# Kernel optimization log

Hardware: AMD Instinct MI355X
Metric: run time of the kernel (lower is better)

Reference implementation:

```python
import jax, jax.numpy as jnp
import numpy as np

B, V, K, DIN, H, DH, OBS, HID = 2048, 3, 32, 256, 8, 64, 128, 256
REP = H * DH
EPS = 1e-6


def _ln(x, g, b):
    mu = x.mean(-1, keepdims=True)
    var = ((x - mu) ** 2).mean(-1, keepdims=True)
    return (x - mu) * jax.lax.rsqrt(var + 1e-5) * g + b


def setup_inputs() -> dict:
    key = jax.random.key(0)
    ks = iter(jax.random.split(key, 32))
    nrm = lambda shape, s=0.05: jax.random.normal(next(ks), shape, jnp.float32) * s
    return {
        'x_anchor': jax.random.normal(next(ks), (B, V, DIN), jnp.float32),
        'x_neighbors': jax.random.normal(next(ks), (B, V, K, DIN), jnp.float32),
        'edge_weights': jax.random.uniform(next(ks), (B, V, K), jnp.float32),
        'g': jax.random.normal(next(ks), (B, OBS), jnp.float32),
        'aW': nrm((V, DIN, REP)), 'ab': jnp.zeros((V, REP)), 'ag': jnp.ones((V, REP)), 'abeta': jnp.zeros((V, REP)),
        'nW': nrm((V, DIN, REP)), 'nb': jnp.zeros((V, REP)), 'ng': jnp.ones((V, REP)), 'nbeta': jnp.zeros((V, REP)),
        'Wq': nrm((V, H, DH, DH)), 'Wk': nrm((V, H, DH, DH)), 'Wv': nrm((V, H, DH, DH)), 'Wo': nrm((V, H, DH, DH)),
        'geom_log_scale': jnp.zeros((V, H)),
        'cWq': nrm((H, DH, DH)), 'cWk': nrm((H, DH, DH)), 'cWv': nrm((H, DH, DH)), 'cWo': nrm((H, DH, DH)),
        'rW1': nrm((OBS, HID)), 'rb1': jnp.zeros((HID,)),
        'rW2': nrm((HID, HID)), 'rb2': jnp.zeros((HID,)),
        'vW': nrm((HID, H * V)), 'vb': jnp.zeros((H * V,)),
        'mW': nrm((HID, H)), 'mb': jnp.zeros((H,)),
        'gW': nrm((HID, H)), 'gb': jnp.zeros((H,)),
    }


def reference(x_anchor, x_neighbors, edge_weights, g, aW, ab, ag, abeta, nW, nb, ng, nbeta,
              Wq, Wk, Wv, Wo, geom_log_scale, cWq, cWk, cWv, cWo,
              rW1, rb1, rW2, rb2, vW, vb, mW, mb, gW, gb):
    # --- per-view encoders (vectorized over V with a leading v axis) ---
    ha = _ln(jnp.einsum('bvi,vio->bvo', x_anchor, aW) + ab, ag, abeta).reshape(B, V, H, DH)
    hn = _ln(jnp.einsum('bvki,vio->bvko', x_neighbors, nW) + nb[:, None, :],
             ng[:, None, :], nbeta[:, None, :]).reshape(B, V, K, H, DH)
    q = jnp.einsum('bvhd,vhde->bvhe', ha, Wq)
    k = jnp.einsum('bvkhd,vhde->bvkhe', hn, Wk)
    vv = jnp.einsum('bvkhd,vhde->bvkhe', hn, Wv)
    sc = jnp.einsum('bvhd,bvkhd->bvhk', q, k) / np.sqrt(DH).astype(np.float32)
    geom = jax.nn.softplus(geom_log_scale)  # [V,H]
    sc = sc + geom[None, :, :, None] * jnp.log(edge_weights[:, :, None, :] + EPS)
    attn = jax.nn.softmax(sc, axis=-1)
    ho = jnp.einsum('bvhk,bvkhd->bvhd', attn, vv)
    ho = jnp.einsum('bvhd,vhde->bvhe', ho, Wo) + ha  # residual
    view_tokens = jnp.transpose(ho, (0, 2, 1, 3))  # [B,H,V,Dh]
    # --- router ---
    hid = jax.nn.gelu(jnp.dot(g, rW1) + rb1, approximate=False)
    hid = jax.nn.gelu(jnp.dot(hid, rW2) + rb2, approximate=False)
    pi = jax.nn.softmax((jnp.dot(hid, vW) + vb).reshape(B, H, V), axis=-1)
    beta = jax.nn.sigmoid((jnp.dot(hid, mW) + mb)[..., None])  # [B,H,1]
    gate = jax.nn.softmax(jnp.dot(hid, gW) + gb, axis=-1)      # [B,H]
    # --- pi-weighted mixture + cross-view interaction with log-pi prior ---
    mix = jnp.einsum('bhv,bhvd->bhd', pi, view_tokens)
    qc = jnp.einsum('bhd,hde->bhe', mix, cWq)
    kc = jnp.einsum('bhvd,hde->bhve', view_tokens, cWk)
    vc = jnp.einsum('bhvd,hde->bhve', view_tokens, cWv)
    s2 = jnp.einsum('bhd,bhvd->bhv', qc, kc) / np.sqrt(DH).astype(np.float32) + jnp.log(pi + EPS)
    a2 = jax.nn.softmax(s2, axis=-1)
    cr = jnp.einsum('bhv,bhvd->bhd', a2, vc)
    cr = jnp.einsum('bhd,hde->bhe', cr, cWo)
    # mode blend + head gating; head_repr kept unflattened [B,H,Dh]
    return gate[..., None] * (beta * cr + (1.0 - beta) * mix)
```

## Files before the change

### kernel.cpp

```cpp
#include <hip/hip_runtime.h>

#define B_   2048
#define V_   3
#define K_   32
#define DIN_ 256
#define H_   8
#define DH_  64
#define REP_ 512

typedef unsigned short u16;
typedef unsigned int   u32;
typedef __bf16 bf8 __attribute__((ext_vector_type(8)));
typedef float  f4  __attribute__((ext_vector_type(4)));

static __device__ __forceinline__ u16 f2bf(float f) {
  union { float f; u32 i; } x; x.f = f;
  u32 r = (x.i + 0x7FFFu + ((x.i >> 16) & 1u)) >> 16;
  return (u16)r;
}
static __device__ __forceinline__ float bf2f(u16 u) {
  union { u32 i; float f; } x; x.i = ((u32)u) << 16;
  return x.f;
}
static __device__ __forceinline__ float bflo(u32 q) {
  union { u32 i; float f; } x; x.i = q << 16; return x.f;
}
static __device__ __forceinline__ float bfhi(u32 q) {
  union { u32 i; float f; } x; x.i = q & 0xffff0000u; return x.f;
}

static __device__ __forceinline__ void gl2lds16(const u16* g, u16* l) {
  __builtin_amdgcn_global_load_lds(
      (const __attribute__((address_space(1))) unsigned int*)(g),
      (__attribute__((address_space(3))) unsigned int*)(l), 16, 0, 0);
}

__global__ __launch_bounds__(256) void k0_prep(
    const float* __restrict__ nW, const float* __restrict__ aW,
    const float* __restrict__ Wv,
    u16* __restrict__ nWt, u16* __restrict__ aWt,
    u16* __restrict__ Wvt)
{
  int id = blockIdx.x * 256 + threadIdx.x;
  if (id < 393216) {
    int v  = id / 131072, r  = id % 131072;
    int kt = r / 16384,   r2 = r % 16384;
    int n  = r2 >> 5;
    int s  = (r2 >> 3) & 3;
    int m  = r2 & 7;
    int c  = s ^ ((n >> 1) & 3);
    int k  = kt * 32 + c * 8 + m;
    int src = (v * 256 + k) * 512 + n;
    nWt[id] = f2bf(nW[src]);
    aWt[id] = f2bf(aW[src]);
  } else {
    int j = id - 393216;
    int vh = j / 4096, r = j % 4096;
    int e = r / 64, d = r % 64;
    int src = (vh * 64 + d) * 64 + e;
    Wvt[j] = f2bf(Wv[src]);
  }
}

__global__ __launch_bounds__(256) void k0_wqk(
    const float* __restrict__ Wq, const float* __restrict__ Wk,
    float* __restrict__ Wqk)
{
  int vh = blockIdx.x, t = threadIdx.x;
  __shared__ float wq[4096], wkT[4096];
  #pragma unroll
  for (int i = 0; i < 16; ++i) {
    int idx = i * 256 + t;
    wq[idx] = Wq[(long)vh * 4096 + idx];
    int e = idx >> 6, c = idx & 63;
    wkT[c * 64 + e] = Wk[(long)vh * 4096 + e * 64 + c];
  }
  __syncthreads();
  int d = t >> 2, e0 = (t & 3) * 16;
  float acc[16];
  #pragma unroll
  for (int j = 0; j < 16; ++j) acc[j] = 0.f;
  for (int c = 0; c < 64; ++c) {
    float a = wq[d * 64 + c];
    const float* wr = &wkT[c * 64 + e0];
    #pragma unroll
    for (int j = 0; j < 16; ++j) acc[j] += a * wr[j];
  }
  #pragma unroll
  for (int j = 0; j < 16; ++j) Wqk[(long)vh * 4096 + d * 64 + e0 + j] = acc[j];
}

__global__ __launch_bounds__(256) void k_tq(
    const float* __restrict__ ha, const float* __restrict__ Wqk,
    float* __restrict__ tB)
{
  __shared__ float hs[512];
  int bv = blockIdx.x, t = threadIdx.x;
  int v = bv % 3;
  hs[t]       = ha[(long)bv * 512 + t];
  hs[256 + t] = ha[(long)bv * 512 + 256 + t];
  __syncthreads();
  int h = t >> 5, e0 = (t & 31) * 2;
  const float* wq = Wqk + ((long)v * 8 + h) * 4096 + e0;
  const float* hv = &hs[h * 64];
  float a0 = 0.f, a1 = 0.f;
  #pragma unroll 4
  for (int d = 0; d < 64; ++d) {
    float x = hv[d];
    float2 wv = *(const float2*)&wq[d * 64];
    a0 += x * wv.x;
    a1 += x * wv.y;
  }
  tB[(long)bv * 512 + h * 64 + e0]     = a0 * 0.125f;
  tB[(long)bv * 512 + h * 64 + e0 + 1] = a1 * 0.125f;
}

union K1Smem {
  struct { u16 A[64 * 256]; u16 B[16384]; } p;
  u16 S[64 * 512];
};

__global__ __launch_bounds__(512, 4) void k1_gemm_ln(
    const float* __restrict__ X,
    const u16*   __restrict__ Wt,
    const float* __restrict__ bias,
    const float* __restrict__ gamma,
    const float* __restrict__ betap,
    u16*   __restrict__ hn,
    float* __restrict__ ha,
    int mode, int b0, int Bc)
{
  __shared__ K1Smem sm;
  const int v = blockIdx.y, blk = blockIdx.x, t = threadIdx.x;
  const int w = t >> 6, l = t & 63, lm = l & 15, lg = l >> 4;
  const int wm = w & 1, wn = w >> 1;

  float bcol[8];
  #pragma unroll
  for (int tn = 0; tn < 8; ++tn) bcol[tn] = bias[v * 512 + wn * 128 + tn * 16 + lm];

  {
    int row = t >> 3;
    int cbase = (t & 7) * 32;
    long grow;
    if (mode == 0) { int b = b0 + blk * 2 + (row >> 5); grow = ((long)(b * 3 + v) * 32 + (row & 31)) * 256; }
    else           { int b = blk * 64 + row;            grow = (long)(b * 3 + v) * 256; }
    const float4* src = (const float4*)(X + grow + cbase);
    int sw = row & 7;
    #pragma unroll
    for (int j = 0; j < 8; ++j) {
      float4 f = src[j];
      int col = cbase + j * 4;
      int c = col >> 3, m = col & 7;
      ushort4 u;
      u.x = f2bf(f.x); u.y = f2bf(f.y); u.z = f2bf(f.z); u.w = f2bf(f.w);
      *(ushort4*)&sm.p.A[row * 256 + ((c ^ sw) << 3) + m] = u;
    }
  }

  f4 acc[2][8];
  #pragma unroll
  for (int i = 0; i < 2; ++i)
    #pragma unroll
    for (int j = 0; j < 8; ++j) { f4 z = {0.f, 0.f, 0.f, 0.f}; acc[i][j] = z; }

  const u16* Wbase = Wt + (long)v * 8 * 16384;
  for (int kt = 0; kt < 8; ++kt) {
    __syncthreads();
    {
      const u16* gp = Wbase + (long)kt * 16384 + t * 8;
      u16* lp = &sm.p.B[t * 8];
      #pragma unroll
      for (int r = 0; r < 4; ++r) gl2lds16(gp + r * 4096, lp + r * 4096);
    }
    __syncthreads();
    bf8 af[2];
    #pragma unroll
    for (int tm = 0; tm < 2; ++tm) {
      int row = wm * 32 + tm * 16 + lm;
      int c = kt * 4 + lg;
      af[tm] = *(const bf8*)&sm.p.A[row * 256 + ((c ^ (row & 7)) << 3)];
    }
    #pragma unroll
    for (int tn = 0; tn < 8; ++tn) {
      int n = wn * 128 + tn * 16 + lm;
      bf8 bv = *(const bf8*)&sm.p.B[n * 32 + ((lg ^ ((n >> 1) & 3)) << 3)];
      acc[0][tn] = __builtin_amdgcn_mfma_f32_16x16x32_bf16(af[0], bv, acc[0][tn], 0, 0, 0);
      acc[1][tn] = __builtin_amdgcn_mfma_f32_16x16x32_bf16(af[1], bv, acc[1][tn], 0, 0, 0);
    }
  }
  __syncthreads();

  #pragma unroll
  for (int tm = 0; tm < 2; ++tm)
    #pragma unroll
    for (int tn = 0; tn < 8; ++tn) {
      int col = wn * 128 + tn * 16 + lm;
      int c = col >> 3, m = col & 7;
      #pragma unroll
      for (int r = 0; r < 4; ++r) {
        int row = wm * 32 + tm * 16 + lg * 4 + r;
        sm.S[row * 512 + ((c ^ (row & 7)) << 3) + m] = f2bf(acc[tm][tn][r] + bcol[tn]);
      }
    }
  __syncthreads();

  {
    int row = t >> 3, ch = t & 7, sw = row & 7;
    float s1 = 0.f, s2 = 0.f;
    #pragma unroll
    for (int j = 0; j < 8; ++j) {
      int c = j * 8 + ch;
      uint4 q = *(const uint4*)&sm.S[row * 512 + ((c ^ sw) << 3)];
      float x0 = bflo(q.x), x1 = bfhi(q.x), x2 = bflo(q.y), x3 = bfhi(q.y);
      float x4 = bflo(q.z), x5 = bfhi(q.z), x6 = bflo(q.w), x7 = bfhi(q.w);
      s1 += ((x0 + x1) + (x2 + x3)) + ((x4 + x5) + (x6 + x7));
      s2 += ((x0*x0 + x1*x1) + (x2*x2 + x3*x3)) + ((x4*x4 + x5*x5) + (x6*x6 + x7*x7));
    }
    #pragma unroll
    for (int d = 1; d < 8; d <<= 1) { s1 += __shfl_xor(s1, d, 64); s2 += __shfl_xor(s2, d, 64); }
    float mu = s1 * (1.f / 512.f);
    float var = s2 * (1.f / 512.f) - mu * mu;
    float rs = rsqrtf(var + 1e-5f);
    #pragma unroll
    for (int j = 0; j < 8; ++j) {
      int c = j * 8 + ch;
      uint4 q = *(const uint4*)&sm.S[row * 512 + ((c ^ sw) << 3)];
      int col0 = c * 8;
      float4 g0 = *(const float4*)&gamma[v * 512 + col0];
      float4 g1 = *(const float4*)&gamma[v * 512 + col0 + 4];
      float4 e0 = *(const float4*)&betap[v * 512 + col0];
      float4 e1 = *(const float4*)&betap[v * 512 + col0 + 4];
      float y0 = (bflo(q.x) - mu) * rs * g0.x + e0.x;
      float y1 = (bfhi(q.x) - mu) * rs * g0.y + e0.y;
      float y2 = (bflo(q.y) - mu) * rs * g0.z + e0.z;
      float y3 = (bfhi(q.y) - mu) * rs * g0.w + e0.w;
      float y4 = (bflo(q.z) - mu) * rs * g1.x + e1.x;
      float y5 = (bfhi(q.z) - mu) * rs * g1.y + e1.y;
      float y6 = (bflo(q.w) - mu) * rs * g1.z + e1.z;
      float y7 = (bfhi(q.w) - mu) * rs * g1.w + e1.w;
      if (mode == 0) {
        uint4 q4;
        q4.x = (u32)f2bf(y0) | ((u32)f2bf(y1) << 16);
        q4.y = (u32)f2bf(y2) | ((u32)f2bf(y3) << 16);
        q4.z = (u32)f2bf(y4) | ((u32)f2bf(y5) << 16);
        q4.w = (u32)f2bf(y6) | ((u32)f2bf(y7) << 16);
        int bl_ = blk * 2 + (row >> 5), krow = row & 31;
        u16* dst = hn + (((long)(v * 8 + j) * Bc + bl_) * 32 + krow) * 64 + ch * 8;
        *(uint4*)dst = q4;
      } else {
        int b = blk * 64 + row;
        float* dst = ha + (long)(b * 3 + v) * 512 + col0;
        float4 w0, w1;
        w0.x = y0; w0.y = y1; w0.z = y2; w0.w = y3;
        w1.x = y4; w1.y = y5; w1.z = y6; w1.w = y7;
        *(float4*)dst = w0;
        *(float4*)(dst + 4) = w1;
      }
    }
  }
}

__global__ __launch_bounds__(512, 4) void k12_fused(
    const float* __restrict__ X,
    const u16*   __restrict__ Wt,
    const float* __restrict__ bias,
    const float* __restrict__ gamma,
    const float* __restrict__ betap,
    const float* __restrict__ ha,
    const u16*   __restrict__ Wvt,
    const float* __restrict__ tB,
    const float* __restrict__ Wo,
    const float* __restrict__ ew,
    const float* __restrict__ gls,
    float* __restrict__ vt)
{
  __shared__ K1Smem sm;
  __shared__ float tS[1024];
  __shared__ float aS[512];
  __shared__ float oS[1024];
  __shared__ float haS[1024];

  const int v = blockIdx.y, blk = blockIdx.x, t = threadIdx.x;
  const int w = t >> 6, l = t & 63, lm = l & 15, lg = l >> 4;
  const int wm = w & 1, wn = w >> 1;

  float bcol[8];
  #pragma unroll
  for (int tn = 0; tn < 8; ++tn) bcol[tn] = bias[v * 512 + wn * 128 + tn * 16 + lm];

  {
    int row = t >> 3;
    int cbase = (t & 7) * 32;
    int b = blk * 2 + (row >> 5);
    long grow = ((long)(b * 3 + v) * 32 + (row & 31)) * 256;
    const float4* src = (const float4*)(X + grow + cbase);
    int sw = row & 7;
    #pragma unroll
    for (int j = 0; j < 8; ++j) {
      float4 f = src[j];
      int col = cbase + j * 4;
      int c = col >> 3, m = col & 7;
      ushort4 u;
      u.x = f2bf(f.x); u.y = f2bf(f.y); u.z = f2bf(f.z); u.w = f2bf(f.w);
      *(ushort4*)&sm.p.A[row * 256 + ((c ^ sw) << 3) + m] = u;
    }
  }
  {
    int b = t >> 8, e = (t & 255) * 2;
    *(float2*)&haS[b * 512 + e] =
        *(const float2*)&ha[((long)(blk * 2 + b) * 3 + v) * 512 + e];
    *(float2*)&tS[b * 512 + e] =
        *(const float2*)&tB[((long)(blk * 2 + b) * 3 + v) * 512 + e];
  }

  f4 acc[2][8];
  #pragma unroll
  for (int i = 0; i < 2; ++i)
    #pragma unroll
    for (int j = 0; j < 8; ++j) { f4 z = {0.f, 0.f, 0.f, 0.f}; acc[i][j] = z; }

  const u16* Wbase = Wt + (long)v * 8 * 16384;
  for (int kt = 0; kt < 8; ++kt) {
    __syncthreads();
    {
      const u16* gp = Wbase + (long)kt * 16384 + t * 8;
      u16* lp = &sm.p.B[t * 8];
      #pragma unroll
      for (int r = 0; r < 4; ++r) gl2lds16(gp + r * 4096, lp + r * 4096);
    }
    __syncthreads();
    bf8 af[2];
    #pragma unroll
    for (int tm = 0; tm < 2; ++tm) {
      int row = wm * 32 + tm * 16 + lm;
      int c = kt * 4 + lg;
      af[tm] = *(const bf8*)&sm.p.A[row * 256 + ((c ^ (row & 7)) << 3)];
    }
    #pragma unroll
    for (int tn = 0; tn < 8; ++tn) {
      int n = wn * 128 + tn * 16 + lm;
      bf8 bv = *(const bf8*)&sm.p.B[n * 32 + ((lg ^ ((n >> 1) & 3)) << 3)];
      acc[0][tn] = __builtin_amdgcn_mfma_f32_16x16x32_bf16(af[0], bv, acc[0][tn], 0, 0, 0);
      acc[1][tn] = __builtin_amdgcn_mfma_f32_16x16x32_bf16(af[1], bv, acc[1][tn], 0, 0, 0);
    }
  }
  __syncthreads();

  #pragma unroll
  for (int tm = 0; tm < 2; ++tm)
    #pragma unroll
    for (int tn = 0; tn < 8; ++tn) {
      int col = wn * 128 + tn * 16 + lm;
      int c = col >> 3, m = col & 7;
      #pragma unroll
      for (int r = 0; r < 4; ++r) {
        int row = wm * 32 + tm * 16 + lg * 4 + r;
        sm.S[row * 512 + ((c ^ (row & 7)) << 3) + m] = f2bf(acc[tm][tn][r] + bcol[tn]);
      }
    }
  __syncthreads();

  {
    int row = t >> 3, ch = t & 7, sw = row & 7;
    float s1 = 0.f, s2 = 0.f;
    #pragma unroll
    for (int j = 0; j < 8; ++j) {
      int c = j * 8 + ch;
      uint4 q = *(const uint4*)&sm.S[row * 512 + ((c ^ sw) << 3)];
      float x0 = bflo(q.x), x1 = bfhi(q.x), x2 = bflo(q.y), x3 = bfhi(q.y);
      float x4 = bflo(q.z), x5 = bfhi(q.z), x6 = bflo(q.w), x7 = bfhi(q.w);
      s1 += ((x0 + x1) + (x2 + x3)) + ((x4 + x5) + (x6 + x7));
      s2 += ((x0*x0 + x1*x1) + (x2*x2 + x3*x3)) + ((x4*x4 + x5*x5) + (x6*x6 + x7*x7));
    }
    #pragma unroll
    for (int d = 1; d < 8; d <<= 1) { s1 += __shfl_xor(s1, d, 64); s2 += __shfl_xor(s2, d, 64); }
    float mu = s1 * (1.f / 512.f);
    float var = s2 * (1.f / 512.f) - mu * mu;
    float rs = rsqrtf(var + 1e-5f);
    #pragma unroll
    for (int j = 0; j < 8; ++j) {
      int c = j * 8 + ch;
      u16* sp = &sm.S[row * 512 + ((c ^ sw) << 3)];
      uint4 q = *(const uint4*)sp;
      int col0 = c * 8;
      float4 g0 = *(const float4*)&gamma[v * 512 + col0];
      float4 g1 = *(const float4*)&gamma[v * 512 + col0 + 4];
      float4 e0 = *(const float4*)&betap[v * 512 + col0];
      float4 e1 = *(const float4*)&betap[v * 512 + col0 + 4];
      float y0 = (bflo(q.x) - mu) * rs * g0.x + e0.x;
      float y1 = (bfhi(q.x) - mu) * rs * g0.y + e0.y;
      float y2 = (bflo(q.y) - mu) * rs * g0.z + e0.z;
      float y3 = (bfhi(q.y) - mu) * rs * g0.w + e0.w;
      float y4 = (bflo(q.z) - mu) * rs * g1.x + e1.x;
      float y5 = (bfhi(q.z) - mu) * rs * g1.y + e1.y;
      float y6 = (bflo(q.w) - mu) * rs * g1.z + e1.z;
      float y7 = (bfhi(q.w) - mu) * rs * g1.w + e1.w;
      uint4 q4;
      q4.x = (u32)f2bf(y0) | ((u32)f2bf(y1) << 16);
      q4.y = (u32)f2bf(y2) | ((u32)f2bf(y3) << 16);
      q4.z = (u32)f2bf(y4) | ((u32)f2bf(y5) << 16);
      q4.w = (u32)f2bf(y6) | ((u32)f2bf(y7) << 16);
      *(uint4*)sp = q4;
    }
  }
  __syncthreads();

  {
    int b = t >> 8, h = (t >> 5) & 7, k = t & 31;
    float x = gls[v * 8 + h];
    float gsc = (x > 20.f) ? x : log1pf(expf(x));
    int r = b * 32 + k, sw = r & 7;
    const float* tb = &tS[(b * 8 + h) * 64];
    float s = 0.f;
    #pragma unroll
    for (int j = 0; j < 8; ++j) {
      int c8 = h * 8 + j;
      uint4 q = *(const uint4*)&sm.S[r * 512 + ((c8 ^ sw) << 3)];
      const float* tj = tb + j * 8;
      s += tj[0] * bflo(q.x) + tj[1] * bfhi(q.x)
         + tj[2] * bflo(q.y) + tj[3] * bfhi(q.y)
         + tj[4] * bflo(q.z) + tj[5] * bfhi(q.z)
         + tj[6] * bflo(q.w) + tj[7] * bfhi(q.w);
    }
    float e_w = ew[((long)(blk * 2 + b) * 3 + v) * 32 + k];
    s += gsc * logf(e_w + 1e-6f);
    float m = s;
    #pragma unroll
    for (int d = 1; d < 32; d <<= 1) m = fmaxf(m, __shfl_xor(m, d, 64));
    float exs = expf(s - m), sum = exs;
    #pragma unroll
    for (int d = 1; d < 32; d <<= 1) sum += __shfl_xor(sum, d, 64);
    aS[(b * 8 + h) * 32 + k] = exs / sum;
  }
  __syncthreads();

  #pragma unroll 1
  for (int i = 0; i < 2; ++i) {
    int p = w * 2 + i, b = p >> 3, h = p & 7;
    const u16* wvg = Wvt + (long)(v * 8 + h) * 4096;
    f4 aV[2][4];
    #pragma unroll
    for (int a = 0; a < 2; ++a)
      #pragma unroll
      for (int j = 0; j < 4; ++j) { f4 z = {0.f, 0.f, 0.f, 0.f}; aV[a][j] = z; }
    #pragma unroll
    for (int ks = 0; ks < 2; ++ks) {
      int ko = ks * 32 + lg * 8;
      bf8 af[2];
      #pragma unroll
      for (int tm = 0; tm < 2; ++tm) {
        int r = b * 32 + tm * 16 + lm;
        int c8 = h * 8 + ks * 4 + lg;
        af[tm] = *(const bf8*)&sm.S[r * 512 + ((c8 ^ (r & 7)) << 3)];
      }
      #pragma unroll
      for (int tn = 0; tn < 4; ++tn) {
        bf8 bv = *(const bf8*)&wvg[(tn * 16 + lm) * 64 + ko];
        #pragma unroll
        for (int tm = 0; tm < 2; ++tm)
          aV[tm][tn] = __builtin_amdgcn_mfma_f32_16x16x32_bf16(af[tm], bv, aV[tm][tn], 0, 0, 0);
      }
    }
    float pp[4] = {0.f, 0.f, 0.f, 0.f};
    #pragma unroll
    for (int tm = 0; tm < 2; ++tm)
      #pragma unroll
      for (int r4 = 0; r4 < 4; ++r4) {
        int k = tm * 16 + lg * 4 + r4;
        float a = aS[p * 32 + k];
        #pragma unroll
        for (int tn = 0; tn < 4; ++tn) pp[tn] += a * aV[tm][tn][r4];
      }
    #pragma unroll
    for (int tn = 0; tn < 4; ++tn) {
      float x = pp[tn];
      x += __shfl_xor(x, 16, 64);
      x += __shfl_xor(x, 32, 64);
      if (l < 16) oS[p * 64 + tn * 16 + lm] = x;
    }
  }
  __syncthreads();

  {
    int h = t >> 6, e = t & 63;
    const float* wo = Wo + (long)(v * 8 + h) * 4096;
    float a0 = haS[h * 64 + e];
    float a1 = haS[512 + h * 64 + e];
    const float* o0 = &oS[h * 64];
    const float* o1 = &oS[512 + h * 64];
    #pragma unroll 4
    for (int d = 0; d < 64; ++d) {
      float wv = wo[d * 64 + e];
      a0 += o0[d] * wv;
      a1 += o1[d] * wv;
    }
    vt[(((long)(blk * 2 + 0) * 8 + h) * 3 + v) * 64 + e] = a0;
    vt[(((long)(blk * 2 + 1) * 8 + h) * 3 + v) * 64 + e] = a1;
  }
}

__global__ __launch_bounds__(256) void k3_router(
    const float* __restrict__ g, const float* __restrict__ rW1, const float* __restrict__ rb1,
    const float* __restrict__ rW2, const float* __restrict__ rb2,
    const float* __restrict__ vW, const float* __restrict__ vb,
    const float* __restrict__ mW, const float* __restrict__ mb,
    const float* __restrict__ gW, const float* __restrict__ gb,
    float* __restrict__ pi, float* __restrict__ beta_o, float* __restrict__ gate_o)
{
  __shared__ float gs[4 * 128], h1[4 * 256], h2[4 * 256], lgt[4 * 40];
  int t = threadIdx.x, bb = blockIdx.x * 4;
  #pragma unroll
  for (int r = 0; r < 2; ++r) { int idx = r * 256 + t; gs[idx] = g[(long)bb * 128 + idx]; }
  __syncthreads();
  {
    int bl = t >> 6, e0 = (t & 63) * 4;
    float acc[4];
    #pragma unroll
    for (int j = 0; j < 4; ++j) acc[j] = rb1[e0 + j];
    for (int i = 0; i < 128; ++i) {
      float gv = gs[bl * 128 + i];
      const float* wr = rW1 + i * 256 + e0;
      #pragma unroll
      for (int j = 0; j < 4; ++j) acc[j] += gv * wr[j];
    }
    #pragma unroll
    for (int j = 0; j < 4; ++j) { float x = acc[j]; h1[bl * 256 + e0 + j] = 0.5f * x * (1.f + erff(x * 0.70710678118f)); }
  }
  __syncthreads();
  {
    int bl = t >> 6, e0 = (t & 63) * 4;
    float acc[4];
    #pragma unroll
    for (int j = 0; j < 4; ++j) acc[j] = rb2[e0 + j];
    for (int i = 0; i < 256; ++i) {
      float hv = h1[bl * 256 + i];
      const float* wr = rW2 + i * 256 + e0;
      #pragma unroll
      for (int j = 0; j < 4; ++j) acc[j] += hv * wr[j];
    }
    #pragma unroll
    for (int j = 0; j < 4; ++j) { float x = acc[j]; h2[bl * 256 + e0 + j] = 0.5f * x * (1.f + erff(x * 0.70710678118f)); }
  }
  __syncthreads();
  if (t < 160) {
    int bl = t / 40, j = t % 40;
    const float* W; float bs; int col, stride;
    if (j < 24)      { W = vW; col = j;      stride = 24; bs = vb[j]; }
    else if (j < 32) { W = mW; col = j - 24; stride = 8;  bs = mb[j - 24]; }
    else             { W = gW; col = j - 32; stride = 8;  bs = gb[j - 32]; }
    float acc = bs;
    for (int i = 0; i < 256; ++i) acc += h2[bl * 256 + i] * W[i * stride + col];
    lgt[bl * 40 + j] = acc;
  }
  __syncthreads();
  if (t < 4) {
    int b = bb + t;
    const float* L = &lgt[t * 40];
    #pragma unroll
    for (int hh = 0; hh < 8; ++hh) {
      float a0 = L[hh * 3], a1 = L[hh * 3 + 1], a2v = L[hh * 3 + 2];
      float m = fmaxf(a0, fmaxf(a1, a2v));
      float x0 = expf(a0 - m), x1 = expf(a1 - m), x2 = expf(a2v - m);
      float inv = 1.f / (x0 + x1 + x2);
      pi[b * 24 + hh * 3 + 0] = x0 * inv;
      pi[b * 24 + hh * 3 + 1] = x1 * inv;
      pi[b * 24 + hh * 3 + 2] = x2 * inv;
      beta_o[b * 8 + hh] = 1.f / (1.f + expf(-L[24 + hh]));
    }
    float m = L[32];
    #pragma unroll
    for (int hh = 1; hh < 8; ++hh) m = fmaxf(m, L[32 + hh]);
    float s = 0.f, ex[8];
    #pragma unroll
    for (int hh = 0; hh < 8; ++hh) { ex[hh] = expf(L[32 + hh] - m); s += ex[hh]; }
    float inv = 1.f / s;
    #pragma unroll
    for (int hh = 0; hh < 8; ++hh) gate_o[b * 8 + hh] = ex[hh] * inv;
  }
}

__global__ __launch_bounds__(256) void k4_cross(
    const float* __restrict__ vtg, const float* __restrict__ pig,
    const float* __restrict__ betag, const float* __restrict__ gateg,
    const float* __restrict__ cWq, const float* __restrict__ cWk,
    const float* __restrict__ cWv, const float* __restrict__ cWo,
    float* __restrict__ out)
{
  __shared__ float smem[12544];
  float* vts   = smem;
  float* mixs  = smem + 6144;
  float* buf1  = smem + 8192;
  float* buf2  = smem + 10240;
  float* a2s   = smem + 12288;
  float* pis   = smem + 12384;
  float* betas = smem + 12480;
  float* gates = smem + 12512;

  int t = threadIdx.x, bblk = blockIdx.x * 4;
  {
    const float4* src = (const float4*)(vtg + (long)bblk * 1536);
    #pragma unroll
    for (int r = 0; r < 6; ++r) ((float4*)vts)[r * 256 + t] = src[r * 256 + t];
    if (t < 96) pis[t] = pig[bblk * 24 + t];
    if (t < 32) { betas[t] = betag[bblk * 8 + t]; gates[t] = gateg[bblk * 8 + t]; }
  }
  __syncthreads();
  int bl = t >> 6, hh = (t >> 3) & 7, e0 = (t & 7) * 8;
  const float* vbh = &vts[(bl * 8 + hh) * 192];
  {
    float p0 = pis[bl * 24 + hh * 3], p1 = pis[bl * 24 + hh * 3 + 1], p2 = pis[bl * 24 + hh * 3 + 2];
    #pragma unroll
    for (int j = 0; j < 8; ++j) {
      int e = e0 + j;
      mixs[(bl * 8 + hh) * 64 + e] = p0 * vbh[e] + p1 * vbh[64 + e] + p2 * vbh[128 + e];
    }
  }
  __syncthreads();
  {
    float acc[8] = {0.f,0.f,0.f,0.f,0.f,0.f,0.f,0.f};
    const float* M = &mixs[(bl * 8 + hh) * 64];
    for (int d = 0; d < 64; ++d) {
      float mv = M[d];
      const float* wr = &cWq[(hh * 64 + d) * 64 + e0];
      #pragma unroll
      for (int j = 0; j < 8; ++j) acc[j] += mv * wr[j];
    }
    #pragma unroll
    for (int j = 0; j < 8; ++j) buf1[(bl * 8 + hh) * 64 + e0 + j] = acc[j] * 0.125f;
  }
  __syncthreads();
  {
    const float* Q = &buf1[(bl * 8 + hh) * 64];
    #pragma unroll
    for (int d2 = 0; d2 < 8; ++d2) {
      const float* wr = &cWk[(hh * 64 + e0 + d2) * 64];
      float a = 0.f;
      for (int e = 0; e < 64; ++e) a += wr[e] * Q[e];
      buf2[(bl * 8 + hh) * 64 + e0 + d2] = a;
    }
  }
  __syncthreads();
  if (t < 32) {
    int b2 = t >> 3, h2 = t & 7;
    const float* Wd = &buf2[(b2 * 8 + h2) * 64];
    const float* vb2 = &vts[(b2 * 8 + h2) * 192];
    float s[3];
    #pragma unroll
    for (int v3 = 0; v3 < 3; ++v3) {
      float a = 0.f;
      for (int d = 0; d < 64; ++d) a += Wd[d] * vb2[v3 * 64 + d];
      s[v3] = a + logf(pis[b2 * 24 + h2 * 3 + v3] + 1e-6f);
    }
    float m = fmaxf(s[0], fmaxf(s[1], s[2]));
    float x0 = expf(s[0] - m), x1 = expf(s[1] - m), x2 = expf(s[2] - m);
    float inv = 1.f / (x0 + x1 + x2);
    a2s[(b2 * 8 + h2) * 3 + 0] = x0 * inv;
    a2s[(b2 * 8 + h2) * 3 + 1] = x1 * inv;
    a2s[(b2 * 8 + h2) * 3 + 2] = x2 * inv;
  }
  __syncthreads();
  {
    float a0 = a2s[(bl * 8 + hh) * 3], a1 = a2s[(bl * 8 + hh) * 3 + 1], a2v = a2s[(bl * 8 + hh) * 3 + 2];
    #pragma unroll
    for (int j = 0; j < 8; ++j) {
      int e = e0 + j;
      buf1[(bl * 8 + hh) * 64 + e] = a0 * vbh[e] + a1 * vbh[64 + e] + a2v * vbh[128 + e];
    }
  }
  __syncthreads();
  {
    float acc[8] = {0.f,0.f,0.f,0.f,0.f,0.f,0.f,0.f};
    const float* Y = &buf1[(bl * 8 + hh) * 64];
    for (int d = 0; d < 64; ++d) {
      float yv = Y[d];
      const float* wr = &cWv[(hh * 64 + d) * 64 + e0];
      #pragma unroll
      for (int j = 0; j < 8; ++j) acc[j] += yv * wr[j];
    }
    #pragma unroll
    for (int j = 0; j < 8; ++j) buf2[(bl * 8 + hh) * 64 + e0 + j] = acc[j];
  }
  __syncthreads();
  {
    float acc[8] = {0.f,0.f,0.f,0.f,0.f,0.f,0.f,0.f};
    const float* C2 = &buf2[(bl * 8 + hh) * 64];
    for (int d = 0; d < 64; ++d) {
      float cv = C2[d];
      const float* wr = &cWo[(hh * 64 + d) * 64 + e0];
      #pragma unroll
      for (int j = 0; j < 8; ++j) acc[j] += cv * wr[j];
    }
    float bt = betas[bl * 8 + hh], gt = gates[bl * 8 + hh];
    const float* M = &mixs[(bl * 8 + hh) * 64];
    #pragma unroll
    for (int j = 0; j < 8; ++j)
      out[((long)(bblk + bl) * 8 + hh) * 64 + e0 + j] = gt * (bt * acc[j] + (1.f - bt) * M[e0 + j]);
  }
}

extern "C" void kernel_launch(void* const* d_in, const int* in_sizes, int n_in,
                              void* d_out, int out_size, void* d_ws, size_t ws_size,
                              hipStream_t stream) {
  const float* x_anchor    = (const float*)d_in[0];
  const float* x_neighbors = (const float*)d_in[1];
  const float* edge_w      = (const float*)d_in[2];
  const float* g           = (const float*)d_in[3];
  const float* aW  = (const float*)d_in[4];
  const float* ab  = (const float*)d_in[5];
  const float* ag  = (const float*)d_in[6];
  const float* abeta = (const float*)d_in[7];
  const float* nW  = (const float*)d_in[8];
  const float* nb  = (const float*)d_in[9];
  const float* ng  = (const float*)d_in[10];
  const float* nbeta = (const float*)d_in[11];
  const float* Wq  = (const float*)d_in[12];
  const float* Wk  = (const float*)d_in[13];
  const float* Wv  = (const float*)d_in[14];
  const float* Wo  = (const float*)d_in[15];
  const float* gls = (const float*)d_in[16];
  const float* cWq = (const float*)d_in[17];
  const float* cWk = (const float*)d_in[18];
  const float* cWv = (const float*)d_in[19];
  const float* cWo = (const float*)d_in[20];
  const float* rW1 = (const float*)d_in[21];
  const float* rb1 = (const float*)d_in[22];
  const float* rW2 = (const float*)d_in[23];
  const float* rb2 = (const float*)d_in[24];
  const float* vW  = (const float*)d_in[25];
  const float* vb  = (const float*)d_in[26];
  const float* mW  = (const float*)d_in[27];
  const float* mb  = (const float*)d_in[28];
  const float* gW  = (const float*)d_in[29];
  const float* gb  = (const float*)d_in[30];

  char* p = (char*)d_ws;
  u16* nWt = (u16*)p;  p += 786432;
  u16* aWt = (u16*)p;  p += 786432;
  u16* Wvt = (u16*)p;  p += 196608;
  float* WqkB = (float*)p; p += 393216;
  float* ha   = (float*)p; p += 12582912;
  float* vtb  = (float*)p; p += 12582912;
  float* tqB  = (float*)p; p += 12582912;
  float* pib  = (float*)p; p += 196608;
  float* betb = (float*)p; p += 65536;
  float* gatb = (float*)p; p += 65536;
  (void)ws_size;

  k0_prep<<<1920, 256, 0, stream>>>(nW, aW, Wv, nWt, aWt, Wvt);
  k0_wqk<<<24, 256, 0, stream>>>(Wq, Wk, WqkB);
  k1_gemm_ln<<<dim3(32, 3), 512, 0, stream>>>(x_anchor, aWt, ab, ag, abeta,
                                              (u16*)nullptr, ha, 1, 0, 2048);
  k_tq<<<6144, 256, 0, stream>>>(ha, WqkB, tqB);
  k3_router<<<512, 256, 0, stream>>>(g, rW1, rb1, rW2, rb2, vW, vb, mW, mb, gW, gb,
                                     pib, betb, gatb);
  k12_fused<<<dim3(1024, 3), 512, 0, stream>>>(x_neighbors, nWt, nb, ng, nbeta,
                                               ha, Wvt, tqB, Wo, edge_w, gls, vtb);
  k4_cross<<<512, 256, 0, stream>>>(vtb, pib, betb, gatb, cWq, cWk, cWv, cWo,
                                    (float*)d_out);
}
```

Baseline: 767.0 us.

## Compute LayerNorm stats from MFMA accumulators in registers, skip bf16 staging pass

Swaps the MFMA operand order so each lane's accumulators hold four consecutive columns of one row. Bias add and the LayerNorm sum and sum-of-squares are then computed in registers, reduced across waves through a small shared buffer, and normalized values are written to shared memory once as bf16. This removes the pre-normalization bf16 store, the two re-read passes and a barrier, and computes statistics in fp32 rather than from bf16-rounded values. It also drops the haS shared buffer (the residual is read directly from global) to reduce LDS use and possibly raise occupancy, and raises the Wo loop unroll.

Result: faster. 732.2 us (-4.5%).

```diff
diff --git a/kernel.cpp b/kernel.cpp
--- a/kernel.cpp
+++ b/kernel.cpp
@@ -278,16 +278,14 @@
   __shared__ K1Smem sm;
   __shared__ float tS[1024];
   __shared__ float aS[512];
-  __shared__ float oS[1024];
-  __shared__ float haS[1024];
+  __shared__ float oSbuf[1024];
+  float* lnP1 = oSbuf;
+  float* lnP2 = oSbuf + 256;
+  float* muRs = oSbuf + 512;
 
   const int v = blockIdx.y, blk = blockIdx.x, t = threadIdx.x;
   const int w = t >> 6, l = t & 63, lm = l & 15, lg = l >> 4;
   const int wm = w & 1, wn = w >> 1;
-
-  float bcol[8];
-  #pragma unroll
-  for (int tn = 0; tn < 8; ++tn) bcol[tn] = bias[v * 512 + wn * 128 + tn * 16 + lm];
 
   {
     int row = t >> 3;
@@ -308,8 +306,6 @@
   }
   {
     int b = t >> 8, e = (t & 255) * 2;
-    *(float2*)&haS[b * 512 + e] =
-        *(const float2*)&ha[((long)(blk * 2 + b) * 3 + v) * 512 + e];
     *(float2*)&tS[b * 512 + e] =
         *(const float2*)&tB[((long)(blk * 2 + b) * 3 + v) * 512 + e];
   }
@@ -341,67 +337,77 @@
     for (int tn = 0; tn < 8; ++tn) {
       int n = wn * 128 + tn * 16 + lm;
       bf8 bv = *(const bf8*)&sm.p.B[n * 32 + ((lg ^ ((n >> 1) & 3)) << 3)];
-      acc[0][tn] = __builtin_amdgcn_mfma_f32_16x16x32_bf16(af[0], bv, acc[0][tn], 0, 0, 0);
-      acc[1][tn] = __builtin_amdgcn_mfma_f32_16x16x32_bf16(af[1], bv, acc[1][tn], 0, 0, 0);
-    }
-  }
-  __syncthreads();
-
-  #pragma unroll
-  for (int tm = 0; tm < 2; ++tm)
+      acc[0][tn] = __builtin_amdgcn_mfma_f32_16x16x32_bf16(bv, af[0], acc[0][tn], 0, 0, 0);
+      acc[1][tn] = __builtin_amdgcn_mfma_f32_16x16x32_bf16(bv, af[1], acc[1][tn], 0, 0, 0);
+    }
+  }
+
+  #pragma unroll
+  for (int tn = 0; tn < 8; ++tn) {
+    float4 bb = *(const float4*)&bias[v * 512 + wn * 128 + tn * 16 + lg * 4];
+    #pragma unroll
+    for (int r = 0; r < 4; ++r) { acc[0][tn][r] += ((const float*)&bb)[r]; acc[1][tn][r] += ((const float*)&bb)[r]; }
+  }
+
+  {
+    #pragma unroll
+    for (int tm = 0; tm < 2; ++tm) {
+      float s1 = 0.f, s2 = 0.f;
+      #pragma unroll
+      for (int tn = 0; tn < 8; ++tn)
+        #pragma unroll
+        for (int r = 0; r < 4; ++r) { float z = acc[tm][tn][r]; s1 += z; s2 += z * z; }
+      s1 += __shfl_xor(s1, 16, 64); s2 += __shfl_xor(s2, 16, 64);
+      s1 += __shfl_xor(s1, 32, 64); s2 += __shfl_xor(s2, 32, 64);
+      if (lg == 0) {
+        int row = wm * 32 + tm * 16 + lm;
+        lnP1[row * 4 + wn] = s1;
+        lnP2[row * 4 + wn] = s2;
+      }
+    }
+  }
+  __syncthreads();
+  if (t < 64) {
+    float p = lnP1[t * 4] + lnP1[t * 4 + 1] + lnP1[t * 4 + 2] + lnP1[t * 4 + 3];
+    float q = lnP2[t * 4] + lnP2[t * 4 + 1] + lnP2[t * 4 + 2] + lnP2[t * 4 + 3];
+    float mu = p * (1.f / 512.f);
+    float var = q * (1.f / 512.f) - mu * mu;
+    muRs[t]      = mu;
+    muRs[64 + t] = rsqrtf(var + 1e-5f);
+  }
+  __syncthreads();
+
+  {
+    float mu0 = muRs[wm * 32 + lm],      rs0 = muRs[64 + wm * 32 + lm];
+    float mu1 = muRs[wm * 32 + 16 + lm], rs1 = muRs[64 + wm * 32 + 16 + lm];
+    int row0 = wm * 32 + lm, row1 = row0 + 16;
+    int sw0 = row0 & 7, sw1 = row1 & 7;
     #pragma unroll
     for (int tn = 0; tn < 8; ++tn) {
-      int col = wn * 128 + tn * 16 + lm;
-      int c = col >> 3, m = col & 7;
-      #pragma unroll
-      for (int r = 0; r < 4; ++r) {
-        int row = wm * 32 + tm * 16 + lg * 4 + r;
-        sm.S[row * 512 + ((c ^ (row & 7)) << 3) + m] = f2bf(acc[tm][tn][r] + bcol[tn]);
+      int col0 = wn * 128 + tn * 16 + lg * 4;
+      int c = col0 >> 3, m0 = col0 & 7;
+      float4 g4 = *(const float4*)&gamma[v * 512 + col0];
+      float4 b4 = *(const float4*)&betap[v * 512 + col0];
+      {
+        float y0 = (acc[0][tn][0] - mu0) * rs0 * g4.x + b4.x;
+        float y1 = (acc[0][tn][1] - mu0) * rs0 * g4.y + b4.y;
+        float y2 = (acc[0][tn][2] - mu0) * rs0 * g4.z + b4.z;
+        float y3 = (acc[0][tn][3] - mu0) * rs0 * g4.w + b4.w;
+        uint2 p;
+        p.x = (u32)f2bf(y0) | ((u32)f2bf(y1) << 16);
+        p.y = (u32)f2bf(y2) | ((u32)f2bf(y3) << 16);
+        *(uint2*)&sm.S[row0 * 512 + ((c ^ sw0) << 3) + m0] = p;
       }
-    }
-  __syncthreads();
-
-  {
-    int row = t >> 3, ch = t & 7, sw = row & 7;
-    float s1 = 0.f, s2 = 0.f;
-    #pragma unroll
-    for (int j = 0; j < 8; ++j) {
-      int c = j * 8 + ch;
-      uint4 q = *(const uint4*)&sm.S[row * 512 + ((c ^ sw) << 3)];
-      float x0 = bflo(q.x), x1 = bfhi(q.x), x2 = bflo(q.y), x3 = bfhi(q.y);
-      float x4 = bflo(q.z), x5 = bfhi(q.z), x6 = bflo(q.w), x7 = bfhi(q.w);
-      s1 += ((x0 + x1) + (x2 + x3)) + ((x4 + x5) + (x6 + x7));
-      s2 += ((x0*x0 + x1*x1) + (x2*x2 + x3*x3)) + ((x4*x4 + x5*x5) + (x6*x6 + x7*x7));
-    }
-    #pragma unroll
-    for (int d = 1; d < 8; d <<= 1) { s1 += __shfl_xor(s1, d, 64); s2 += __shfl_xor(s2, d, 64); }
-    float mu = s1 * (1.f / 512.f);
-    float var = s2 * (1.f / 512.f) - mu * mu;
-    float rs = rsqrtf(var + 1e-5f);
-    #pragma unroll
-    for (int j = 0; j < 8; ++j) {
-      int c = j * 8 + ch;
-      u16* sp = &sm.S[row * 512 + ((c ^ sw) << 3)];
-      uint4 q = *(const uint4*)sp;
-      int col0 = c * 8;
-      float4 g0 = *(const float4*)&gamma[v * 512 + col0];
-      float4 g1 = *(const float4*)&gamma[v * 512 + col0 + 4];
-      float4 e0 = *(const float4*)&betap[v * 512 + col0];
-      float4 e1 = *(const float4*)&betap[v * 512 + col0 + 4];
-      float y0 = (bflo(q.x) - mu) * rs * g0.x + e0.x;
-      float y1 = (bfhi(q.x) - mu) * rs * g0.y + e0.y;
-      float y2 = (bflo(q.y) - mu) * rs * g0.z + e0.z;
-      float y3 = (bfhi(q.y) - mu) * rs * g0.w + e0.w;
-      float y4 = (bflo(q.z) - mu) * rs * g1.x + e1.x;
-      float y5 = (bfhi(q.z) - mu) * rs * g1.y + e1.y;
-      float y6 = (bflo(q.w) - mu) * rs * g1.z + e1.z;
-      float y7 = (bfhi(q.w) - mu) * rs * g1.w + e1.w;
-      uint4 q4;
-      q4.x = (u32)f2bf(y0) | ((u32)f2bf(y1) << 16);
-      q4.y = (u32)f2bf(y2) | ((u32)f2bf(y3) << 16);
-      q4.z = (u32)f2bf(y4) | ((u32)f2bf(y5) << 16);
-      q4.w = (u32)f2bf(y6) | ((u32)f2bf(y7) << 16);
-      *(uint4*)sp = q4;
+      {
+        float y0 = (acc[1][tn][0] - mu1) * rs1 * g4.x + b4.x;
+        float y1 = (acc[1][tn][1] - mu1) * rs1 * g4.y + b4.y;
+        float y2 = (acc[1][tn][2] - mu1) * rs1 * g4.z + b4.z;
+        float y3 = (acc[1][tn][3] - mu1) * rs1 * g4.w + b4.w;
+        uint2 p;
+        p.x = (u32)f2bf(y0) | ((u32)f2bf(y1) << 16);
+        p.y = (u32)f2bf(y2) | ((u32)f2bf(y3) << 16);
+        *(uint2*)&sm.S[row1 * 512 + ((c ^ sw1) << 3) + m0] = p;
+      }
     }
   }
   __syncthreads();
@@ -477,7 +483,7 @@
       float x = pp[tn];
       x += __shfl_xor(x, 16, 64);
       x += __shfl_xor(x, 32, 64);
-      if (l < 16) oS[p * 64 + tn * 16 + lm] = x;
+      if (l < 16) oSbuf[p * 64 + tn * 16 + lm] = x;
     }
   }
   __syncthreads();
@@ -485,11 +491,11 @@
   {
     int h = t >> 6, e = t & 63;
     const float* wo = Wo + (long)(v * 8 + h) * 4096;
-    float a0 = haS[h * 64 + e];
-    float a1 = haS[512 + h * 64 + e];
-    const float* o0 = &oS[h * 64];
-    const float* o1 = &oS[512 + h * 64];
-    #pragma unroll 4
+    float a0 = ha[((long)(blk * 2 + 0) * 3 + v) * 512 + h * 64 + e];
+    float a1 = ha[((long)(blk * 2 + 1) * 3 + v) * 512 + h * 64 + e];
+    const float* o0 = &oSbuf[h * 64];
+    const float* o1 = &oSbuf[512 + h * 64];
+    #pragma unroll 8
     for (int d = 0; d < 64; ++d) {
       float wv = wo[d * 64 + e];
       a0 += o0[d] * wv;
```
